# Optimization experiments

Hardware: AMD Instinct MI355X
Metric: run time of the kernel (lower is better)

## Reference

```python
import jax, jax.numpy as jnp
import numpy as np
from jax import lax

B, E = 32, 8
O, I, K = 192, 192, 3
H, W = 56, 56
PAD = 1  # static 'same' padding for k=3, s=1, d=1


def setup_inputs() -> dict:
    key = jax.random.key(0)
    k1, k2, k3, k4 = jax.random.split(key, 4)
    x = jax.random.normal(k1, (B, I, H, W), dtype=jnp.float32)
    routing_weights = jax.random.uniform(k2, (B, E), dtype=jnp.float32)
    weight = jax.random.normal(k3, (E, O * I * K * K), dtype=jnp.float32) * 0.05
    bias = jax.random.normal(k4, (E, O), dtype=jnp.float32) * 0.05
    return {"x": x, "routing_weights": routing_weights, "weight": weight, "bias": bias}


def _condconv(x, routing_weights, weight, bias):
    # Mix expert weights per sample: [B, E] @ [E, O*I*K*K] -> [B, O, I, K, K]
    w = jnp.matmul(routing_weights, weight).reshape(B, O, I, K, K)
    b = jnp.matmul(routing_weights, bias)  # [B, O]

    def conv_one(xi, wi):
        # xi: [I, H, W], wi: [O, I, K, K] -> [O, H, W]
        out = lax.conv_general_dilated(
            xi[None], wi, window_strides=(1, 1),
            padding=[(PAD, PAD), (PAD, PAD)],
            dimension_numbers=("NCHW", "OIHW", "NCHW"))
        return out[0]

    out = jax.vmap(conv_one)(x, w)  # [B, O, H, W]
    return out + b[:, :, None, None]


def reference(x, routing_weights, weight, bias):
    return _condconv(x, routing_weights, weight, bias)
```

## Files before the change

kernel.cpp:

```cpp
#include <hip/hip_runtime.h>
#include <hip/hip_bf16.h>

typedef __attribute__((ext_vector_type(8))) short bf16x8;
typedef __attribute__((ext_vector_type(4))) float f32x4;

#define B_ 32
#define E_ 8
#define O_ 192
#define I_ 192
#define H_ 56
#define W_ 56
#define HW_ 3136
#define IK_ (I_ * 9)
#define WSZ_ (O_ * IK_)

#define WT_E ((size_t)B_ * 9 * 24 * 192 * 8)
#define XT_E ((size_t)B_ * HW_ * 192)

static __device__ __forceinline__ unsigned short f2bf(float v) {
    __hip_bfloat16 h = __float2bfloat16(v);
    return *reinterpret_cast<unsigned short*>(&h);
}
static __device__ __forceinline__ float bf2f(unsigned short u) {
    __hip_bfloat16 h = *reinterpret_cast<__hip_bfloat16*>(&u);
    return __bfloat162float(h);
}

__global__ __launch_bounds__(256) void mix_split_w(
    const float* __restrict__ r, const float* __restrict__ Wt,
    const float* __restrict__ bias, unsigned short* __restrict__ whi,
    unsigned short* __restrict__ wlo, float* __restrict__ bmix) {
    __shared__ float rs[B_ * E_];
    int t = threadIdx.x;
    rs[t] = r[t];
    __syncthreads();
    int gid = blockIdx.x * 256 + t;

    if (gid < B_ * O_) {
        int b = gid / O_, o = gid - b * O_;
        float acc = 0.f;
#pragma unroll
        for (int e = 0; e < E_; ++e)
            acc = fmaf(rs[b * E_ + e], bias[e * O_ + o], acc);
        bmix[gid] = acc;
    }
    if (gid >= O_ * I_) return;
    int o = gid / I_, i = gid - o * I_;

    float we[E_][9];
#pragma unroll
    for (int e = 0; e < E_; ++e)
#pragma unroll
        for (int s = 0; s < 9; ++s)
            we[e][s] = Wt[(size_t)e * WSZ_ + (size_t)gid * 9 + s];

    for (int b = 0; b < B_; ++b) {
#pragma unroll
        for (int s = 0; s < 9; ++s) {
            float v = 0.f;
#pragma unroll
            for (int e = 0; e < E_; ++e) v = fmaf(rs[b * E_ + e], we[e][s], v);
            unsigned short h = f2bf(v);
            unsigned short l = f2bf(v - bf2f(h));
            size_t oidx =
                ((((size_t)(b * 9 + s)) * 24 + (i >> 3)) * 192 + o) * 8 +
                (i & 7);
            whi[oidx] = h;
            wlo[oidx] = l;
        }
    }
}

__global__ __launch_bounds__(256) void split_x(
    const float* __restrict__ x, unsigned short* __restrict__ xhi,
    unsigned short* __restrict__ xlo) {
    __shared__ float tile[64][65];
    int t = threadIdx.x;
    int tx = t & 63, ty = t >> 6;
    int b = blockIdx.z, i0 = blockIdx.y * 64, hw0 = blockIdx.x * 64;
    const float* xb = x + ((size_t)b * I_ + i0) * HW_ + hw0;
#pragma unroll
    for (int k = 0; k < 16; ++k) {
        int il = ty * 16 + k;
        tile[il][tx] = xb[(size_t)il * HW_ + tx];
    }
    __syncthreads();
#pragma unroll
    for (int k = 0; k < 16; ++k) {
        int hwl = ty * 16 + k;
        float v = tile[tx][hwl];
        unsigned short h = f2bf(v);
        unsigned short l = f2bf(v - bf2f(h));
        size_t oidx = ((size_t)b * HW_ + hw0 + hwl) * I_ + i0 + tx;
        xhi[oidx] = h;
        xlo[oidx] = l;
    }
}

__global__ __launch_bounds__(128, 2) void conv_mfma(
    const unsigned short* __restrict__ xhi,
    const unsigned short* __restrict__ xlo,
    const unsigned short* __restrict__ whi,
    const unsigned short* __restrict__ wlo,
    const float* __restrict__ bmix, float* __restrict__ out) {
    __shared__ __align__(16) unsigned char xs[2 * 14848];

    const int t = threadIdx.x;
    const int lane = t & 63, wv = t >> 6;
    const int lc = lane & 15, g = lane >> 4;
    const int h0 = blockIdx.x * 2;
    const int ob = blockIdx.y * 96 + wv * 48;
    const int b = blockIdx.z;

    int rowbase[7];
#pragma unroll
    for (int f = 0; f < 7; ++f) {
        int ploc = f * 16 + lc;
        int hh = (ploc >= 56) ? 1 : 0;
        int wl = ploc - 56 * hh;
        rowbase[f] = hh * 58 + wl;
    }

    f32x4 acc[3][7];
#pragma unroll
    for (int mi = 0; mi < 3; ++mi)
#pragma unroll
        for (int f = 0; f < 7; ++f) acc[mi][f] = (f32x4){0.f, 0.f, 0.f, 0.f};

    for (int icb = 0; icb < 6; ++icb) {
        __syncthreads();
#pragma unroll
        for (int it = 0; it < 8; ++it) {
            int idx = it * 128 + t;
            if (idx < 928) {
                int row = idx >> 2, c = idx & 3;
                int rr = row / 58, ww = row - rr * 58;
                int h = h0 - 1 + rr, w = ww - 1;
                bf16x8 vh = (bf16x8){0, 0, 0, 0, 0, 0, 0, 0};
                bf16x8 vl = (bf16x8){0, 0, 0, 0, 0, 0, 0, 0};
                if ((unsigned)h < (unsigned)H_ && (unsigned)w < (unsigned)W_) {
                    size_t goff =
                        ((size_t)(b * HW_ + h * W_ + w)) * 192 + icb * 32 +
                        c * 8;
                    vh = *(const bf16x8*)(xhi + goff);
                    vl = *(const bf16x8*)(xlo + goff);
                }
                int off = row * 64 + ((c ^ ((row >> 1) & 3)) << 4);
                *(bf16x8*)(xs + off) = vh;
                *(bf16x8*)(xs + 14848 + off) = vl;
            }
        }
        __syncthreads();

#pragma unroll
        for (int s = 0; s < 9; ++s) {
            const int dh = s / 3, dw = s - dh * 3;
            bf16x8 ah[3], al[3];
#pragma unroll
            for (int mi = 0; mi < 3; ++mi) {
                size_t aidx =
                    ((((size_t)(b * 9 + s)) * 24 + icb * 4 + g) * 192 +
                     (ob + mi * 16 + lc)) * 8;
                ah[mi] = *(const bf16x8*)(whi + aidx);
                al[mi] = *(const bf16x8*)(wlo + aidx);
            }
#pragma unroll
            for (int f = 0; f < 7; ++f) {
                int row = rowbase[f] + dh * 58 + dw;
                int off = row * 64 + (((g ^ (row >> 1)) & 3) << 4);
                bf16x8 bh = *(const bf16x8*)(xs + off);
                bf16x8 bl = *(const bf16x8*)(xs + 14848 + off);
#pragma unroll
                for (int mi = 0; mi < 3; ++mi) {
                    acc[mi][f] = __builtin_amdgcn_mfma_f32_16x16x32_bf16(
                        ah[mi], bh, acc[mi][f], 0, 0, 0);
                    acc[mi][f] = __builtin_amdgcn_mfma_f32_16x16x32_bf16(
                        ah[mi], bl, acc[mi][f], 0, 0, 0);
                    acc[mi][f] = __builtin_amdgcn_mfma_f32_16x16x32_bf16(
                        al[mi], bh, acc[mi][f], 0, 0, 0);
                }
            }
        }
    }

#pragma unroll
    for (int mi = 0; mi < 3; ++mi) {
#pragma unroll
        for (int j = 0; j < 4; ++j) {
            int o = ob + mi * 16 + g * 4 + j;
            float bs = bmix[b * O_ + o];
            float* op = out + ((size_t)(b * O_ + o)) * HW_;
#pragma unroll
            for (int f = 0; f < 7; ++f) {
                int ploc = f * 16 + lc;
                int hh = (ploc >= 56) ? 1 : 0;
                int wl = ploc - 56 * hh;
                op[(h0 + hh) * W_ + wl] = acc[mi][f][j] + bs;
            }
        }
    }
}

__global__ __launch_bounds__(256, 2) void condconv_fp32(
    const float* __restrict__ x, const float* __restrict__ wsrc,
    const float* __restrict__ r, const float* __restrict__ bias,
    float* __restrict__ out) {
    __shared__ float xsf[16][6][58];
    __shared__ float wsm[16 * 9][68];

    const int t = threadIdx.x;
    const int wg = t & 7;
    const int hg = (t >> 3) & 1;
    const int og = t >> 4;
    const int h0 = blockIdx.x * 4;
    const int o0 = blockIdx.y * 64;
    const int b = blockIdx.z;
    const float* xb = x + (size_t)b * I_ * H_ * W_;

    float rb[E_];
#pragma unroll
    for (int e = 0; e < E_; ++e) rb[e] = r[b * E_ + e];

    float acc[4][2][7];
#pragma unroll
    for (int oo = 0; oo < 4; ++oo)
#pragma unroll
        for (int hh = 0; hh < 2; ++hh)
#pragma unroll
            for (int ww = 0; ww < 7; ++ww) acc[oo][hh][ww] = 0.f;

    for (int ic = 0; ic < I_; ic += 16) {
        __syncthreads();
        for (int idx = t; idx < 16 * 6 * 58; idx += 256) {
            int ch = idx / (6 * 58);
            int rem = idx - ch * (6 * 58);
            int rr = rem / 58;
            int cc = rem - rr * 58;
            int hgl = h0 - 1 + rr;
            int wgl = cc - 1;
            float v = 0.f;
            if ((unsigned)hgl < H_ && (unsigned)wgl < W_)
                v = xb[(size_t)(ic + ch) * (H_ * W_) + hgl * W_ + wgl];
            ((float*)xsf)[idx] = v;
        }
        for (int idx = t; idx < 64 * 144; idx += 256) {
            int o = idx / 144;
            int ikl = idx - o * 144;
            float v = 0.f;
#pragma unroll
            for (int e = 0; e < E_; ++e)
                v = fmaf(rb[e],
                         wsrc[(size_t)e * WSZ_ + (size_t)(o0 + o) * IK_ +
                              ic * 9 + ikl],
                         v);
            wsm[ikl][o] = v;
        }
        __syncthreads();
        for (int i = 0; i < 16; ++i) {
#pragma unroll
            for (int kh = 0; kh < 3; ++kh) {
                float xr[2][9];
#pragma unroll
                for (int hh = 0; hh < 2; ++hh)
#pragma unroll
                    for (int c = 0; c < 9; ++c)
                        xr[hh][c] = xsf[i][hg * 2 + hh + kh][wg * 7 + c];
#pragma unroll
                for (int kw = 0; kw < 3; ++kw) {
                    float4 wv = *(const float4*)&wsm[i * 9 + kh * 3 + kw][og * 4];
                    float wreg[4] = {wv.x, wv.y, wv.z, wv.w};
#pragma unroll
                    for (int oo = 0; oo < 4; ++oo)
#pragma unroll
                        for (int hh = 0; hh < 2; ++hh)
#pragma unroll
                            for (int ww = 0; ww < 7; ++ww)
                                acc[oo][hh][ww] = fmaf(wreg[oo], xr[hh][kw + ww],
                                                       acc[oo][hh][ww]);
                }
            }
        }
    }
#pragma unroll
    for (int oo = 0; oo < 4; ++oo) {
        int o = o0 + og * 4 + oo;
        float bs = 0.f;
#pragma unroll
        for (int e = 0; e < E_; ++e) bs = fmaf(rb[e], bias[e * O_ + o], bs);
        float* ob = out + ((size_t)b * O_ + o) * (H_ * W_);
#pragma unroll
        for (int hh = 0; hh < 2; ++hh) {
            int h = h0 + hg * 2 + hh;
#pragma unroll
            for (int ww = 0; ww < 7; ++ww)
                ob[h * W_ + wg * 7 + ww] = acc[oo][hh][ww] + bs;
        }
    }
}

extern "C" void kernel_launch(void* const* d_in, const int* in_sizes, int n_in,
                              void* d_out, int out_size, void* d_ws,
                              size_t ws_size, hipStream_t stream) {
    const float* x = (const float*)d_in[0];
    const float* r = (const float*)d_in[1];
    const float* Wt = (const float*)d_in[2];
    const float* bias = (const float*)d_in[3];
    float* out = (float*)d_out;

    const size_t need = 2 * WT_E * 2 + 2 * XT_E * 2 + (size_t)B_ * O_ * 4;

    if (ws_size >= need) {
        unsigned char* p = (unsigned char*)d_ws;
        unsigned short* whi = (unsigned short*)p; p += WT_E * 2;
        unsigned short* wlo = (unsigned short*)p; p += WT_E * 2;
        unsigned short* xh = (unsigned short*)p; p += XT_E * 2;
        unsigned short* xl = (unsigned short*)p; p += XT_E * 2;
        float* bmix = (float*)p;

        mix_split_w<<<(O_ * I_) / 256, 256, 0, stream>>>(r, Wt, bias, whi, wlo,
                                                         bmix);
        split_x<<<dim3(HW_ / 64, I_ / 64, B_), 256, 0, stream>>>(x, xh, xl);
        conv_mfma<<<dim3(H_ / 2, 2, B_), 128, 0, stream>>>(xh, xl, whi, wlo,
                                                           bmix, out);
    } else {
        condconv_fp32<<<dim3(H_ / 4, O_ / 64, B_), 256, 0, stream>>>(x, Wt, r,
                                                                     bias, out);
    }
}
```

Before: 496.8 us.

## Switch split-bf16 triple MFMA to single fp16 MFMA with pipelined staging

Drops the hi/lo bf16 split, which cost three MFMAs per product, and uses a single fp16 MFMA on fp16-converted activations and mixed weights. This removes two thirds of the matrix math and halves the workspace traffic. The conv kernel now runs 256 threads over 4 output rows and double-buffers the LDS input tile, with register-staged prefetch two stages ahead. The expert-mix kernel is parallelized over batch as well, and x is relaid out per 32-channel block. Accuracy drops to fp16 precision (about 11 mantissa bits) with fp32 accumulation, so tolerance may become a concern.

```diff
diff --git a/kernel.cpp b/kernel.cpp
--- a/kernel.cpp
+++ b/kernel.cpp
@@ -1,8 +1,8 @@
 #include <hip/hip_runtime.h>
-#include <hip/hip_bf16.h>
-
-typedef __attribute__((ext_vector_type(8))) short bf16x8;
-typedef __attribute__((ext_vector_type(4))) float f32x4;
+#include <hip/hip_fp16.h>
+
+using f16x8 = __attribute__((ext_vector_type(8))) _Float16;
+using f32x4 = __attribute__((ext_vector_type(4))) float;
 
 #define B_ 32
 #define E_ 8
@@ -11,72 +11,56 @@
 #define H_ 56
 #define W_ 56
 #define HW_ 3136
-#define IK_ (I_ * 9)
+#define IK_ 1728
 #define WSZ_ (O_ * IK_)
 
-#define WT_E ((size_t)B_ * 9 * 24 * 192 * 8)
-#define XT_E ((size_t)B_ * HW_ * 192)
-
-static __device__ __forceinline__ unsigned short f2bf(float v) {
-    __hip_bfloat16 h = __float2bfloat16(v);
-    return *reinterpret_cast<unsigned short*>(&h);
-}
-static __device__ __forceinline__ float bf2f(unsigned short u) {
-    __hip_bfloat16 h = *reinterpret_cast<__hip_bfloat16*>(&u);
-    return __bfloat162float(h);
-}
-
-__global__ __launch_bounds__(256) void mix_split_w(
+#define WT_E ((size_t)B_ * 9 * 24 * O_ * 8)
+#define XT_E ((size_t)B_ * 6 * HW_ * 32)
+#define S_STRIDE 36864
+#define ICB_STRIDE 100352
+
+__global__ __launch_bounds__(256) void mix_w(
     const float* __restrict__ r, const float* __restrict__ Wt,
-    const float* __restrict__ bias, unsigned short* __restrict__ whi,
-    unsigned short* __restrict__ wlo, float* __restrict__ bmix) {
-    __shared__ float rs[B_ * E_];
-    int t = threadIdx.x;
-    rs[t] = r[t];
-    __syncthreads();
-    int gid = blockIdx.x * 256 + t;
-
-    if (gid < B_ * O_) {
-        int b = gid / O_, o = gid - b * O_;
-        float acc = 0.f;
+    const float* __restrict__ bias, _Float16* __restrict__ wT,
+    float* __restrict__ bmix) {
+    int gid = blockIdx.x * 256 + threadIdx.x;
+    int b = gid / (O_ * I_);
+    int rem = gid - b * (O_ * I_);
+    int o = rem / I_;
+    int i = rem - o * I_;
+
+    float rb[E_];
+#pragma unroll
+    for (int e = 0; e < E_; ++e) rb[e] = r[b * E_ + e];
+
+    float acc[9];
+#pragma unroll
+    for (int s = 0; s < 9; ++s) acc[s] = 0.f;
+#pragma unroll
+    for (int e = 0; e < E_; ++e) {
+        const float* wp = Wt + (size_t)e * WSZ_ + (size_t)rem * 9;
+#pragma unroll
+        for (int s = 0; s < 9; ++s) acc[s] = fmaf(rb[e], wp[s], acc[s]);
+    }
+    size_t base =
+        (((size_t)(b * 9) * 24 + (i >> 3)) * O_ + o) * 8 + (i & 7);
+#pragma unroll
+    for (int s = 0; s < 9; ++s)
+        wT[base + (size_t)s * S_STRIDE] = (_Float16)acc[s];
+
+    if (i == 0) {
+        float bacc = 0.f;
 #pragma unroll
         for (int e = 0; e < E_; ++e)
-            acc = fmaf(rs[b * E_ + e], bias[e * O_ + o], acc);
-        bmix[gid] = acc;
-    }
-    if (gid >= O_ * I_) return;
-    int o = gid / I_, i = gid - o * I_;
-
-    float we[E_][9];
-#pragma unroll
-    for (int e = 0; e < E_; ++e)
-#pragma unroll
-        for (int s = 0; s < 9; ++s)
-            we[e][s] = Wt[(size_t)e * WSZ_ + (size_t)gid * 9 + s];
-
-    for (int b = 0; b < B_; ++b) {
-#pragma unroll
-        for (int s = 0; s < 9; ++s) {
-            float v = 0.f;
-#pragma unroll
-            for (int e = 0; e < E_; ++e) v = fmaf(rs[b * E_ + e], we[e][s], v);
-            unsigned short h = f2bf(v);
-            unsigned short l = f2bf(v - bf2f(h));
-            size_t oidx =
-                ((((size_t)(b * 9 + s)) * 24 + (i >> 3)) * 192 + o) * 8 +
-                (i & 7);
-            whi[oidx] = h;
-            wlo[oidx] = l;
-        }
-    }
-}
-
-__global__ __launch_bounds__(256) void split_x(
-    const float* __restrict__ x, unsigned short* __restrict__ xhi,
-    unsigned short* __restrict__ xlo) {
+            bacc = fmaf(rb[e], bias[e * O_ + o], bacc);
+        bmix[b * O_ + o] = bacc;
+    }
+}
+
+__global__ __launch_bounds__(256) void xsplit(const float* __restrict__ x,
+                                              _Float16* __restrict__ xT) {
     __shared__ float tile[64][65];
-    int t = threadIdx.x;
-    int tx = t & 63, ty = t >> 6;
+    int t = threadIdx.x, tx = t & 63, ty = t >> 6;
     int b = blockIdx.z, i0 = blockIdx.y * 64, hw0 = blockIdx.x * 64;
     const float* xb = x + ((size_t)b * I_ + i0) * HW_ + hw0;
 #pragma unroll
@@ -85,40 +69,72 @@
         tile[il][tx] = xb[(size_t)il * HW_ + tx];
     }
     __syncthreads();
+    int i = i0 + tx;
 #pragma unroll
     for (int k = 0; k < 16; ++k) {
         int hwl = ty * 16 + k;
-        float v = tile[tx][hwl];
-        unsigned short h = f2bf(v);
-        unsigned short l = f2bf(v - bf2f(h));
-        size_t oidx = ((size_t)b * HW_ + hw0 + hwl) * I_ + i0 + tx;
-        xhi[oidx] = h;
-        xlo[oidx] = l;
-    }
-}
-
-__global__ __launch_bounds__(128, 2) void conv_mfma(
-    const unsigned short* __restrict__ xhi,
-    const unsigned short* __restrict__ xlo,
-    const unsigned short* __restrict__ whi,
-    const unsigned short* __restrict__ wlo,
+        xT[(((size_t)b * 6 + (i >> 5)) * HW_ + hw0 + hwl) * 32 + (i & 31)] =
+            (_Float16)tile[tx][hwl];
+    }
+}
+
+__global__ __launch_bounds__(256, 3) void conv_f16(
+    const _Float16* __restrict__ xT, const _Float16* __restrict__ wT,
     const float* __restrict__ bmix, float* __restrict__ out) {
-    __shared__ __align__(16) unsigned char xs[2 * 14848];
+    __shared__ __align__(16) unsigned char xs[2][22272];
 
     const int t = threadIdx.x;
     const int lane = t & 63, wv = t >> 6;
     const int lc = lane & 15, g = lane >> 4;
-    const int h0 = blockIdx.x * 2;
-    const int ob = blockIdx.y * 96 + wv * 48;
+    const int h0 = blockIdx.x * 4;
+    const int ob = blockIdx.y * 96 + (wv >> 1) * 48;
+    const int pbase = (wv & 1) * 112;
     const int b = blockIdx.z;
 
     int rowbase[7];
 #pragma unroll
     for (int f = 0; f < 7; ++f) {
-        int ploc = f * 16 + lc;
-        int hh = (ploc >= 56) ? 1 : 0;
-        int wl = ploc - 56 * hh;
-        rowbase[f] = hh * 58 + wl;
+        int ploc = pbase + f * 16 + lc;
+        rowbase[f] = (ploc / 56) * 58 + (ploc % 56);
+    }
+
+    int soff[6];
+    int qoff[6];
+#pragma unroll
+    for (int q = 0; q < 6; ++q) {
+        int idx = q * 256 + t;
+        if (idx < 1392) {
+            int row = idx >> 2, c = idx & 3;
+            int rr = row / 58, ww = row - rr * 58;
+            soff[q] = row * 64 + (((c ^ (row >> 1)) & 3) << 4);
+            int h = h0 - 1 + rr, w = ww - 1;
+            if ((unsigned)h < (unsigned)H_ && (unsigned)w < (unsigned)W_)
+                qoff[q] = (((b * 6) * HW_ + h * W_ + w) << 5) + c * 8;
+            else
+                qoff[q] = -1;
+        } else {
+            soff[q] = -1;
+            qoff[q] = -1;
+        }
+    }
+
+    f16x8 stg[6];
+    const f16x8 zero8 = (f16x8){0, 0, 0, 0, 0, 0, 0, 0};
+
+#define LOADSTAGE(icb)                                                      \
+    {                                                                       \
+        _Pragma("unroll") for (int q = 0; q < 6; ++q) {                     \
+            stg[q] = (qoff[q] >= 0)                                         \
+                         ? *(const f16x8*)(xT + qoff[q] +                   \
+                                           (icb) * ICB_STRIDE)              \
+                         : zero8;                                           \
+        }                                                                   \
+    }
+#define WRITESTAGE(buf)                                                     \
+    {                                                                       \
+        _Pragma("unroll") for (int q = 0; q < 6; ++q) {                     \
+            if (soff[q] >= 0) *(f16x8*)(xs[buf] + soff[q]) = stg[q];        \
+        }                                                                   \
     }
 
     f32x4 acc[3][7];
@@ -127,59 +143,40 @@
 #pragma unroll
         for (int f = 0; f < 7; ++f) acc[mi][f] = (f32x4){0.f, 0.f, 0.f, 0.f};
 
-    for (int icb = 0; icb < 6; ++icb) {
-        __syncthreads();
-#pragma unroll
-        for (int it = 0; it < 8; ++it) {
-            int idx = it * 128 + t;
-            if (idx < 928) {
-                int row = idx >> 2, c = idx & 3;
-                int rr = row / 58, ww = row - rr * 58;
-                int h = h0 - 1 + rr, w = ww - 1;
-                bf16x8 vh = (bf16x8){0, 0, 0, 0, 0, 0, 0, 0};
-                bf16x8 vl = (bf16x8){0, 0, 0, 0, 0, 0, 0, 0};
-                if ((unsigned)h < (unsigned)H_ && (unsigned)w < (unsigned)W_) {
-                    size_t goff =
-                        ((size_t)(b * HW_ + h * W_ + w)) * 192 + icb * 32 +
-                        c * 8;
-                    vh = *(const bf16x8*)(xhi + goff);
-                    vl = *(const bf16x8*)(xlo + goff);
-                }
-                int off = row * 64 + ((c ^ ((row >> 1) & 3)) << 4);
-                *(bf16x8*)(xs + off) = vh;
-                *(bf16x8*)(xs + 14848 + off) = vl;
-            }
-        }
-        __syncthreads();
-
+    LOADSTAGE(0);
+    WRITESTAGE(0);
+    LOADSTAGE(1);
+    __syncthreads();
+
+    for (int k = 0; k < 6; ++k) {
+        const int buf = k & 1;
 #pragma unroll
         for (int s = 0; s < 9; ++s) {
             const int dh = s / 3, dw = s - dh * 3;
-            bf16x8 ah[3], al[3];
-#pragma unroll
-            for (int mi = 0; mi < 3; ++mi) {
-                size_t aidx =
-                    ((((size_t)(b * 9 + s)) * 24 + icb * 4 + g) * 192 +
-                     (ob + mi * 16 + lc)) * 8;
-                ah[mi] = *(const bf16x8*)(whi + aidx);
-                al[mi] = *(const bf16x8*)(wlo + aidx);
-            }
+            f16x8 ah[3];
+#pragma unroll
+            for (int mi = 0; mi < 3; ++mi)
+                ah[mi] = *(const f16x8*)(wT +
+                                         ((((size_t)(b * 9 + s) * 24 +
+                                            k * 4 + g) *
+                                               O_ +
+                                           (ob + mi * 16 + lc))
+                                          << 3));
 #pragma unroll
             for (int f = 0; f < 7; ++f) {
                 int row = rowbase[f] + dh * 58 + dw;
                 int off = row * 64 + (((g ^ (row >> 1)) & 3) << 4);
-                bf16x8 bh = *(const bf16x8*)(xs + off);
-                bf16x8 bl = *(const bf16x8*)(xs + 14848 + off);
-#pragma unroll
-                for (int mi = 0; mi < 3; ++mi) {
-                    acc[mi][f] = __builtin_amdgcn_mfma_f32_16x16x32_bf16(
-                        ah[mi], bh, acc[mi][f], 0, 0, 0);
-                    acc[mi][f] = __builtin_amdgcn_mfma_f32_16x16x32_bf16(
-                        ah[mi], bl, acc[mi][f], 0, 0, 0);
-                    acc[mi][f] = __builtin_amdgcn_mfma_f32_16x16x32_bf16(
-                        al[mi], bh, acc[mi][f], 0, 0, 0);
-                }
+                f16x8 bv = *(const f16x8*)(xs[buf] + off);
+#pragma unroll
+                for (int mi = 0; mi < 3; ++mi)
+                    acc[mi][f] = __builtin_amdgcn_mfma_f32_16x16x32_f16(
+                        ah[mi], bv, acc[mi][f], 0, 0, 0);
             }
+        }
+        if (k < 5) {
+            WRITESTAGE(buf ^ 1);
+            if (k < 4) LOADSTAGE(k + 2);
+            __syncthreads();
         }
     }
 
@@ -189,16 +186,16 @@
         for (int j = 0; j < 4; ++j) {
             int o = ob + mi * 16 + g * 4 + j;
             float bs = bmix[b * O_ + o];
-            float* op = out + ((size_t)(b * O_ + o)) * HW_;
+            float* op = out + ((size_t)(b * O_ + o)) * HW_ + (size_t)h0 * W_;
 #pragma unroll
             for (int f = 0; f < 7; ++f) {
-                int ploc = f * 16 + lc;
-                int hh = (ploc >= 56) ? 1 : 0;
-                int wl = ploc - 56 * hh;
-                op[(h0 + hh) * W_ + wl] = acc[mi][f][j] + bs;
+                int ploc = pbase + f * 16 + lc;
+                op[ploc] = acc[mi][f][j] + bs;
             }
         }
     }
+#undef LOADSTAGE
+#undef WRITESTAGE
 }
 
 __global__ __launch_bounds__(256, 2) void condconv_fp32(
@@ -207,20 +204,13 @@
     float* __restrict__ out) {
     __shared__ float xsf[16][6][58];
     __shared__ float wsm[16 * 9][68];
-
     const int t = threadIdx.x;
-    const int wg = t & 7;
-    const int hg = (t >> 3) & 1;
-    const int og = t >> 4;
-    const int h0 = blockIdx.x * 4;
-    const int o0 = blockIdx.y * 64;
-    const int b = blockIdx.z;
+    const int wg = t & 7, hg = (t >> 3) & 1, og = t >> 4;
+    const int h0 = blockIdx.x * 4, o0 = blockIdx.y * 64, b = blockIdx.z;
     const float* xb = x + (size_t)b * I_ * H_ * W_;
-
     float rb[E_];
 #pragma unroll
     for (int e = 0; e < E_; ++e) rb[e] = r[b * E_ + e];
-
     float acc[4][2][7];
 #pragma unroll
     for (int oo = 0; oo < 4; ++oo)
@@ -228,24 +218,19 @@
         for (int hh = 0; hh < 2; ++hh)
 #pragma unroll
             for (int ww = 0; ww < 7; ++ww) acc[oo][hh][ww] = 0.f;
-
     for (int ic = 0; ic < I_; ic += 16) {
         __syncthreads();
         for (int idx = t; idx < 16 * 6 * 58; idx += 256) {
-            int ch = idx / (6 * 58);
-            int rem = idx - ch * (6 * 58);
-            int rr = rem / 58;
-            int cc = rem - rr * 58;
-            int hgl = h0 - 1 + rr;
-            int wgl = cc - 1;
+            int ch = idx / (6 * 58), rem = idx - ch * (6 * 58);
+            int rr = rem / 58, cc = rem - rr * 58;
+            int hgl = h0 - 1 + rr, wgl = cc - 1;
             float v = 0.f;
             if ((unsigned)hgl < H_ && (unsigned)wgl < W_)
                 v = xb[(size_t)(ic + ch) * (H_ * W_) + hgl * W_ + wgl];
             ((float*)xsf)[idx] = v;
         }
         for (int idx = t; idx < 64 * 144; idx += 256) {
-            int o = idx / 144;
-            int ikl = idx - o * 144;
+            int o = idx / 144, ikl = idx - o * 144;
             float v = 0.f;
 #pragma unroll
             for (int e = 0; e < E_; ++e)
@@ -267,7 +252,8 @@
                         xr[hh][c] = xsf[i][hg * 2 + hh + kh][wg * 7 + c];
 #pragma unroll
                 for (int kw = 0; kw < 3; ++kw) {
-                    float4 wv = *(const float4*)&wsm[i * 9 + kh * 3 + kw][og * 4];
+                    float4 wv =
+                        *(const float4*)&wsm[i * 9 + kh * 3 + kw][og * 4];
                     float wreg[4] = {wv.x, wv.y, wv.z, wv.w};
 #pragma unroll
                     for (int oo = 0; oo < 4; ++oo)
@@ -275,8 +261,9 @@
                         for (int hh = 0; hh < 2; ++hh)
 #pragma unroll
                             for (int ww = 0; ww < 7; ++ww)
-                                acc[oo][hh][ww] = fmaf(wreg[oo], xr[hh][kw + ww],
-                                                       acc[oo][hh][ww]);
+                                acc[oo][hh][ww] =
+                                    fmaf(wreg[oo], xr[hh][kw + ww],
+                                         acc[oo][hh][ww]);
                 }
             }
         }
@@ -307,21 +294,19 @@
     const float* bias = (const float*)d_in[3];
     float* out = (float*)d_out;
 
-    const size_t need = 2 * WT_E * 2 + 2 * XT_E * 2 + (size_t)B_ * O_ * 4;
+    const size_t need = WT_E * 2 + XT_E * 2 + (size_t)B_ * O_ * 4;
 
     if (ws_size >= need) {
         unsigned char* p = (unsigned char*)d_ws;
-        unsigned short* whi = (unsigned short*)p; p += WT_E * 2;
-        unsigned short* wlo = (unsigned short*)p; p += WT_E * 2;
-        unsigned short* xh = (unsigned short*)p; p += XT_E * 2;
-        unsigned short* xl = (unsigned short*)p; p += XT_E * 2;
+        _Float16* wT = (_Float16*)p;
+        p += WT_E * 2;
+        _Float16* xT = (_Float16*)p;
+        p += XT_E * 2;
         float* bmix = (float*)p;
 
-        mix_split_w<<<(O_ * I_) / 256, 256, 0, stream>>>(r, Wt, bias, whi, wlo,
-                                                         bmix);
-        split_x<<<dim3(HW_ / 64, I_ / 64, B_), 256, 0, stream>>>(x, xh, xl);
-        conv_mfma<<<dim3(H_ / 2, 2, B_), 128, 0, stream>>>(xh, xl, whi, wlo,
-                                                           bmix, out);
+        mix_w<<<(B_ * O_ * I_) / 256, 256, 0, stream>>>(r, Wt, bias, wT, bmix);
+        xsplit<<<dim3(HW_ / 64, I_ / 64, B_), 256, 0, stream>>>(x, xT);
+        conv_f16<<<dim3(H_ / 4, 2, B_), 256, 0, stream>>>(xT, wT, bmix, out);
     } else {
         condconv_fp32<<<dim3(H_ / 4, O_ / 64, B_), 256, 0, stream>>>(x, Wt, r,
                                                                      bias, out);
```

After: 499.0 us. No clear change (+0.5%).
